# Kernel tuning notes

Measured on AMD Instinct MI355X. Metric: run time of the kernel, lower is better.

Reference implementation:

```python
import jax, jax.numpy as jnp
import numpy as np

DIM = 1024
HEADS = 16
HEAD_DIM = DIM // HEADS
HIDDEN = 4096
EPS = 1e-5


def _layer_norm(x, w, b):
    mu = jnp.mean(x, axis=-1, keepdims=True)
    var = jnp.var(x, axis=-1, keepdims=True)
    return (x - mu) * jax.lax.rsqrt(var + EPS) * w + b


def setup_inputs() -> dict:
    key = jax.random.key(0)
    ks = jax.random.split(key, 16)
    s = lambda fan_in: 1.0 / np.sqrt(fan_in)
    return {
        "x": jax.random.normal(ks[0], (8, 1024, DIM), dtype=jnp.float32),
        "ln1_w": jnp.ones((DIM,), jnp.float32),
        "ln1_b": jnp.zeros((DIM,), jnp.float32),
        "qkv_w": jax.random.uniform(ks[1], (3 * DIM, DIM), jnp.float32, -s(DIM), s(DIM)),
        "qkv_b": jax.random.uniform(ks[2], (3 * DIM,), jnp.float32, -s(DIM), s(DIM)),
        "out_w": jax.random.uniform(ks[3], (DIM, DIM), jnp.float32, -s(DIM), s(DIM)),
        "out_b": jax.random.uniform(ks[4], (DIM,), jnp.float32, -s(DIM), s(DIM)),
        "ln2_w": jnp.ones((DIM,), jnp.float32),
        "ln2_b": jnp.zeros((DIM,), jnp.float32),
        "fc1_w": jax.random.uniform(ks[5], (HIDDEN, DIM), jnp.float32, -s(DIM), s(DIM)),
        "fc1_b": jax.random.uniform(ks[6], (HIDDEN,), jnp.float32, -s(DIM), s(DIM)),
        "fc2_w": jax.random.uniform(ks[7], (DIM, HIDDEN), jnp.float32, -s(HIDDEN), s(HIDDEN)),
        "fc2_b": jax.random.uniform(ks[8], (DIM,), jnp.float32, -s(HIDDEN), s(HIDDEN)),
    }


def reference(x, ln1_w, ln1_b, qkv_w, qkv_b, out_w, out_b,
              ln2_w, ln2_b, fc1_w, fc1_b, fc2_w, fc2_b):
    B, S, D = x.shape
    # --- attention sub-block (pre-LN) ---
    h = _layer_norm(x, ln1_w, ln1_b)
    qkv = h @ qkv_w.T + qkv_b                              # [B,S,3D]
    qkv = qkv.reshape(B, S, 3, HEADS, HEAD_DIM)
    q, k, v = qkv[:, :, 0], qkv[:, :, 1], qkv[:, :, 2]     # [B,S,H,hd]
    scores = jnp.einsum('bqhd,bkhd->bhqk', q, k) / np.sqrt(HEAD_DIM)
    attn = jax.nn.softmax(scores, axis=-1)
    o = jnp.einsum('bhqk,bkhd->bqhd', attn, v).reshape(B, S, D)
    x = x + (o @ out_w.T + out_b)
    # --- MLP sub-block (pre-LN) ---
    h = _layer_norm(x, ln2_w, ln2_b)
    h = jax.nn.gelu(h @ fc1_w.T + fc1_b, approximate=False)
    x = x + (h @ fc2_w.T + fc2_b)
    return x
```

## Files before the change

kernel.cpp:

```cpp
#include <hip/hip_runtime.h>
#include <hip/hip_bf16.h>

typedef unsigned short u16;
typedef __bf16 bf16x8 __attribute__((ext_vector_type(8)));
typedef float f32x4 __attribute__((ext_vector_type(4)));
typedef u16 u16x8 __attribute__((ext_vector_type(8)));
typedef unsigned u32x2 __attribute__((ext_vector_type(2)));

#define LOG2E 1.4426950408889634f
#define QSCALE 0.18033688011112042f

template <int V> struct ic { static constexpr int v = V; };

__device__ __forceinline__ float fast_exp2(float x) {
#if __has_builtin(__builtin_amdgcn_exp2f)
  return __builtin_amdgcn_exp2f(x);
#else
  return exp2f(x);
#endif
}

__device__ __forceinline__ u16 f2bf(float f) {
  union { float f; unsigned u; } c; c.f = f;
  unsigned r = c.u + 0x7fffu + ((c.u >> 16) & 1u);
  return (u16)(r >> 16);
}

__device__ __forceinline__ unsigned pk_bf16(float a, float b) {
#if __has_builtin(__builtin_amdgcn_cvt_pk_bf16_f32)
  typedef __bf16 bf16x2_t __attribute__((ext_vector_type(2)));
  union { bf16x2_t v; unsigned u; } c;
  c.v = __builtin_amdgcn_cvt_pk_bf16_f32(a, b);
  return c.u;
#else
  return (unsigned)f2bf(a) | ((unsigned)f2bf(b) << 16);
#endif
}

__device__ __forceinline__ unsigned pk_bf16_fast(float a, float b) {
#if __has_builtin(__builtin_amdgcn_cvt_pk_bf16_f32)
  return pk_bf16(a, b);
#else
  union { float f; unsigned u; } ca, cb;
  ca.f = a; cb.f = b;
  return __builtin_amdgcn_perm(cb.u, ca.u, 0x07060302u);
#endif
}

__device__ __forceinline__ float gelu_f(float v) {
  float z = 0.7978845608f * v + 0.0356774081f * (v * v * v);
  float e = fast_exp2(z * 2.885390082f);
  float t = 1.0f - 2.0f * __builtin_amdgcn_rcpf(e + 1.0f);
  return 0.5f * v * (1.0f + t);
}

__device__ __forceinline__ void async16(const void* g, void* l) {
  __builtin_amdgcn_global_load_lds(
      (const __attribute__((address_space(1))) void*)g,
      (__attribute__((address_space(3))) void*)l, 16, 0, 0);
}

#define CFENCE asm volatile("" ::: "memory")
#define VMCNT(N) do { asm volatile("s_waitcnt vmcnt(" #N ")" ::: "memory"); \
                      __builtin_amdgcn_sched_barrier(0); } while (0)

__global__ __launch_bounds__(256) void cvt4_kernel(
    const float* __restrict__ s0, const float* __restrict__ s1,
    const float* __restrict__ s2, const float* __restrict__ s3,
    u16* __restrict__ d0, u16* __restrict__ d1,
    u16* __restrict__ d2, u16* __restrict__ d3) {
  int i = blockIdx.x * 256 + threadIdx.x;
  const float* s; u16* d; int off;
  if (i < 786432)       { s = s0; d = d0; off = i; }
  else if (i < 1048576) { s = s1; d = d1; off = i - 786432; }
  else if (i < 2097152) { s = s2; d = d2; off = i - 1048576; }
  else                  { s = s3; d = d3; off = i - 2097152; }
  float4 v = ((const float4*)s)[off];
  ushort4 o;
  o.x = f2bf(v.x); o.y = f2bf(v.y); o.z = f2bf(v.z); o.w = f2bf(v.w);
  ((ushort4*)d)[off] = o;
}

__global__ __launch_bounds__(256) void ln_kernel(const float* __restrict__ x,
                                                 const float* __restrict__ w,
                                                 const float* __restrict__ b,
                                                 u16* __restrict__ out) {
  int row = blockIdx.x;
  int tid = threadIdx.x;
  int lane = tid & 63, wave = tid >> 6;
  float4 v = ((const float4*)(x + (size_t)row * 1024))[tid];
  float s = v.x + v.y + v.z + v.w;
  float s2 = v.x*v.x + v.y*v.y + v.z*v.z + v.w*v.w;
  #pragma unroll
  for (int off = 1; off < 64; off <<= 1) {
    s += __shfl_xor(s, off, 64);
    s2 += __shfl_xor(s2, off, 64);
  }
  __shared__ float red[8];
  if (lane == 0) { red[wave] = s; red[4 + wave] = s2; }
  __syncthreads();
  float st = red[0] + red[1] + red[2] + red[3];
  float s2t = red[4] + red[5] + red[6] + red[7];
  float mu = st * (1.0f / 1024.0f);
  float var = s2t * (1.0f / 1024.0f) - mu * mu;
  float rs = rsqrtf(var + 1e-5f);
  float4 wv = ((const float4*)w)[tid];
  float4 bv = ((const float4*)b)[tid];
  ushort4 o;
  o.x = f2bf((v.x - mu) * rs * wv.x + bv.x);
  o.y = f2bf((v.y - mu) * rs * wv.y + bv.y);
  o.z = f2bf((v.z - mu) * rs * wv.z + bv.z);
  o.w = f2bf((v.w - mu) * rs * wv.w + bv.w);
  ((ushort4*)(out + (size_t)row * 1024))[tid] = o;
}

template <int EPI, int BM, int BN, int NBLOG2>
__global__ __launch_bounds__(512, 2) void gemm8(const u16* __restrict__ A,
                                                const u16* __restrict__ B,
                                                const float* __restrict__ bias,
                                                void* __restrict__ Cout,
                                                const float* __restrict__ resid,
                                                int M, int N, int K) {
  (void)M;
  constexpr int FMH = BM / 64;
  constexpr int FNH = BN / 128;
  constexpr int LA = BM / 128;
  constexpr int LB = BN / 128;
  constexpr int STEADY = LA + LB;
  __shared__ u16 As[2][BM * 64];
  __shared__ u16 Bs[2][BN * 64];
  const int tid = threadIdx.x;
  const int lane = tid & 63, wave = tid >> 6;
  const int wr = wave & 1, wc = wave >> 1;
  const int l15 = lane & 15, l4 = lane >> 4;
  const int nt = K >> 6;

  int m0, n0;
  if constexpr (NBLOG2 < 0) {
    m0 = blockIdx.y * BM; n0 = blockIdx.x * BN;
  } else {
    const int id = blockIdx.x;
    const int xcd = id & 7, slot = id >> 3;
    m0 = ((slot >> NBLOG2) * 8 + xcd) * BM;
    n0 = (slot & ((1 << NBLOG2) - 1)) * BN;
  }

  const int srow = lane >> 3;
  const int sg = (lane & 7) ^ srow;
  const u16* Ab = A + (size_t)(m0 + srow) * K + sg * 8;
  const u16* Bb = B + (size_t)(n0 + srow) * K + sg * 8;

  auto stageA = [&](int tile, int half, int wb) {
    if (tile >= nt) return;
    #pragma unroll
    for (int t = 0; t < LA; t++) {
      const int r0 = half * (BM / 2) + wave * (BM / 16) + t * 8;
      async16(Ab + (size_t)r0 * K + tile * 64, &As[wb][r0 * 64]);
    }
  };
  auto stageB = [&](int tile, int half, int wb) {
    if (tile >= nt) return;
    #pragma unroll
    for (int t = 0; t < LB; t++) {
      const int r0 = half * (BN / 2) + wave * (BN / 16) + t * 8;
      async16(Bb + (size_t)r0 * K + tile * 64, &Bs[wb][r0 * 64]);
    }
  };

  f32x4 acc[2][FMH][2][FNH];
  #pragma unroll
  for (int a = 0; a < 2; a++)
    #pragma unroll
    for (int f = 0; f < FMH; f++)
      #pragma unroll
      for (int c = 0; c < 2; c++)
        #pragma unroll
        for (int g = 0; g < FNH; g++) {
          f32x4 z = {0.f, 0.f, 0.f, 0.f};
          acc[a][f][c][g] = z;
        }

  auto phase = [&](auto qa_, auto qb_, int rb, auto stage) {
    constexpr int qa = decltype(qa_)::v;
    constexpr int qb = decltype(qb_)::v;
    bf16x8 af[FMH][2], bfr[FNH][2];
    #pragma unroll
    for (int f = 0; f < FMH; f++)
      #pragma unroll
      for (int ks = 0; ks < 2; ks++) {
        const int row = qa * (BM / 2) + wr * (BM / 4) + f * 16 + l15;
        const int sl = (ks * 4 + l4) ^ (l15 & 7);
        af[f][ks] = *(const bf16x8*)&As[rb][row * 64 + sl * 8];
      }
    #pragma unroll
    for (int f = 0; f < FNH; f++)
      #pragma unroll
      for (int ks = 0; ks < 2; ks++) {
        const int col = qb * (BN / 2) + wc * (BN / 8) + f * 16 + l15;
        const int sl = (ks * 4 + l4) ^ (l15 & 7);
        bfr[f][ks] = *(const bf16x8*)&Bs[rb][col * 64 + sl * 8];
      }
    stage();
    CFENCE;
    __builtin_amdgcn_s_barrier();
    asm volatile("s_waitcnt lgkmcnt(0)" ::: "memory");
    __builtin_amdgcn_sched_barrier(0);
    __builtin_amdgcn_s_setprio(1);
    #pragma unroll
    for (int f = 0; f < FMH; f++)
      #pragma unroll
      for (int g = 0; g < FNH; g++)
        #pragma unroll
        for (int ks = 0; ks < 2; ks++)
          acc[qa][f][qb][g] = __builtin_amdgcn_mfma_f32_16x16x32_bf16(
              af[f][ks], bfr[g][ks], acc[qa][f][qb][g], 0, 0, 0);
    __builtin_amdgcn_s_setprio(0);
    __builtin_amdgcn_sched_barrier(0);
  };

  auto endphase = [&](int mode) {
    if (mode == 1) {
      if constexpr (STEADY == 4) VMCNT(4); else VMCNT(3);
    } else if (mode == 2) {
      VMCNT(0);
    }
    CFENCE;
    __builtin_amdgcn_s_barrier();
  };

  stageA(0, 0, 0); stageB(0, 0, 0); stageA(0, 1, 0); stageB(0, 1, 0);
  stageA(1, 0, 1); stageB(1, 0, 1);
  if constexpr (STEADY == 4) VMCNT(4); else VMCNT(3);
  CFENCE;
  __builtin_amdgcn_s_barrier();

  const int niter = nt >> 1;
  for (int it = 0; it < niter; ++it) {
    const int T = 2 * it;
    const int f4 = (T + 2 < nt) ? 1 : 2;
    const int f8 = (T + 3 < nt) ? 1 : 2;
    phase(ic<0>{}, ic<0>{}, 0, [&]{ stageA(T + 1, 1, 1); }); endphase(0);
    phase(ic<0>{}, ic<1>{}, 0, [&]{ stageB(T + 1, 1, 1); }); endphase(0);
    phase(ic<1>{}, ic<0>{}, 0, [&]{ stageA(T + 2, 0, 0); }); endphase(0);
    phase(ic<1>{}, ic<1>{}, 0, [&]{ stageB(T + 2, 0, 0); }); endphase(f4);
    phase(ic<0>{}, ic<0>{}, 1, [&]{ stageA(T + 2, 1, 0); }); endphase(0);
    phase(ic<0>{}, ic<1>{}, 1, [&]{ stageB(T + 2, 1, 0); }); endphase(0);
    phase(ic<1>{}, ic<0>{}, 1, [&]{ stageA(T + 3, 0, 1); }); endphase(0);
    phase(ic<1>{}, ic<1>{}, 1, [&]{ stageB(T + 3, 0, 1); }); endphase(f8);
  }

  float bv[2][FNH];
  #pragma unroll
  for (int qb = 0; qb < 2; qb++)
    #pragma unroll
    for (int fn = 0; fn < FNH; fn++)
      bv[qb][fn] = bias[n0 + qb * (BN / 2) + wc * (BN / 8) + fn * 16 + l15];

  #pragma unroll
  for (int qa = 0; qa < 2; qa++)
    #pragma unroll
    for (int fm = 0; fm < FMH; fm++) {
      const size_t row0 =
          (size_t)(m0 + qa * (BM / 2) + wr * (BM / 4) + fm * 16 + l4 * 4);
      #pragma unroll
      for (int r = 0; r < 4; r += 2)
        #pragma unroll
        for (int qb = 0; qb < 2; qb++)
          #pragma unroll
          for (int fn = 0; fn < FNH; fn++) {
            const int col = n0 + qb * (BN / 2) + wc * (BN / 8) + fn * 16 + l15;
            float v0 = acc[qa][fm][qb][fn][r] + bv[qb][fn];
            float v1 = acc[qa][fm][qb][fn][r + 1] + bv[qb][fn];
            if (EPI == 1) { v0 = gelu_f(v0); v1 = gelu_f(v1); }
            if (EPI == 3) {
              float sc = (col < 1024) ? QSCALE : 1.0f;
              v0 *= sc; v1 *= sc;
            }
            const size_t off0 = (row0 + r) * (size_t)N + col;
            const size_t off1 = (row0 + r + 1) * (size_t)N + col;
            if (EPI == 2) {
              ((float*)Cout)[off0] = v0 + resid[off0];
              ((float*)Cout)[off1] = v1 + resid[off1];
            } else {
              unsigned pk = pk_bf16(v0, v1);
              ((u16*)Cout)[off0] = (u16)pk;
              ((u16*)Cout)[off1] = (u16)(pk >> 16);
            }
          }
    }
}

__global__ __launch_bounds__(256) void vtrans_kernel(const u16* __restrict__ qkv,
                                                     u16* __restrict__ vtg) {
  const int sc = blockIdx.x, h = blockIdx.y, b = blockIdx.z;
  const int tid = threadIdx.x;
  __shared__ u16 t[64][72];
  const u16* vp = qkv + ((size_t)b * 1024) * 3072 + h * 64 + 2048;
  #pragma unroll
  for (int it = 0; it < 2; it++) {
    int idx = it * 256 + tid;
    int row = idx >> 3, g = idx & 7;
    *(u16x8*)&t[row][g * 8] =
        *(const u16x8*)(vp + (size_t)(sc * 64 + row) * 3072 + g * 8);
  }
  __syncthreads();
  u16* dst = vtg + ((size_t)(b * 16 + h) * 64) * 1024;
  #pragma unroll
  for (int it = 0; it < 2; it++) {
    int idx = it * 256 + tid;
    int d = idx >> 3, g = idx & 7;
    u16x8 o;
    #pragma unroll
    for (int j = 0; j < 8; j++) o[j] = t[g * 8 + j][d];
    *(u16x8*)(dst + (size_t)d * 1024 + sc * 64 + g * 8) = o;
  }
}

__global__ __launch_bounds__(256) void attn_kernel(const u16* __restrict__ qkv,
                                                   const u16* __restrict__ vtg,
                                                   u16* __restrict__ obuf) {
  const int S = 1024, QKV = 3072;
  const int id = blockIdx.x;
  const int qt = id >> 7, hb = id & 127;
  const int h = hb & 15, b = hb >> 4;
  const int tid = threadIdx.x, lane = tid & 63, wave = tid >> 6;
  const int l15 = lane & 15, l4 = lane >> 4;
  const size_t tok0 = (size_t)b * S;
  const u16* qp = qkv + tok0 * QKV + h * 64;
  const u16* kp = qp + 1024;
  const u16* vtp = vtg + (size_t)(b * 16 + h) * 64 * 1024;
  const int q0 = qt * 128;

  __shared__ u16 Ks[128 * 64];
  __shared__ u16 Vt[64 * 128];
  __shared__ u16 Ps[4][16 * 136];

  const u16* qrow = qp + (size_t)(q0 + wave * 16 + l15) * QKV;
  bf16x8 qf[2][2];
  #pragma unroll
  for (int qs = 0; qs < 2; qs++)
    #pragma unroll
    for (int kb = 0; kb < 2; kb++)
      qf[qs][kb] = *(const bf16x8*)(qrow + (size_t)qs * 64 * QKV + kb * 32 + l4 * 8);

  bf16x8 ones;
  #pragma unroll
  for (int j = 0; j < 8; j++) ones[j] = (__bf16)1.0f;

  const int krow = lane >> 3;
  const int klg = (lane & 7) ^ (lane >> 3);
  const int vrow_i = lane >> 4;
  const int vpg = lane & 15;

  f32x4 oacc[2][4], lacc[2];
  #pragma unroll
  for (int qs = 0; qs < 2; qs++) {
    #pragma unroll
    for (int ct = 0; ct < 4; ct++) {
      f32x4 z = {0.f, 0.f, 0.f, 0.f};
      oacc[qs][ct] = z;
    }
    f32x4 z = {0.f, 0.f, 0.f, 0.f};
    lacc[qs] = z;
  }

  for (int j0 = 0; j0 < S; j0 += 128) {
    __syncthreads();
    #pragma unroll
    for (int t = 0; t < 4; t++) {
      int e = wave * 4 + t;
      async16(kp + (size_t)(j0 + e * 8 + krow) * QKV + klg * 8, Ks + e * 512);
    }
    #pragma unroll
    for (int t = 0; t < 4; t++) {
      int e = wave * 4 + t;
      int row = e * 4 + vrow_i;
      int lg = vpg ^ (row & 15);
      async16(vtp + (size_t)row * 1024 + j0 + lg * 8, Vt + e * 512);
    }
    __syncthreads();

    #pragma unroll
    for (int qs = 0; qs < 2; qs++) {
      f32x4 s[8];
      #pragma unroll
      for (int tg = 0; tg < 8; tg++) {
        f32x4 z = {0.f, 0.f, 0.f, 0.f};
        s[tg] = z;
        #pragma unroll
        for (int kb = 0; kb < 2; kb++) {
          int pg = (kb * 4 + l4) ^ (l15 & 7);
          bf16x8 kf = *(const bf16x8*)&Ks[(tg * 16 + l15) * 64 + pg * 8];
          s[tg] = __builtin_amdgcn_mfma_f32_16x16x32_bf16(kf, qf[qs][kb], s[tg], 0, 0, 0);
        }
      }

      #pragma unroll
      for (int tg = 0; tg < 8; tg++)
        #pragma unroll
        for (int r = 0; r < 4; r++)
          s[tg][r] = fast_exp2(s[tg][r]);

      #pragma unroll
      for (int tg = 0; tg < 8; tg++) {
        u32x2 pr;
        pr[0] = pk_bf16_fast(s[tg][0], s[tg][1]);
        pr[1] = pk_bf16_fast(s[tg][2], s[tg][3]);
        *(u32x2*)&Ps[wave][l15 * 136 + tg * 16 + l4 * 4] = pr;
      }
      bf16x8 pf[4];
      #pragma unroll
      for (int kb = 0; kb < 4; kb++)
        pf[kb] = *(const bf16x8*)&Ps[wave][l15 * 136 + kb * 32 + l4 * 8];

      #pragma unroll
      for (int kb = 0; kb < 4; kb++) {
        #pragma unroll
        for (int ct = 0; ct < 4; ct++) {
          int pg = (kb * 4 + l4) ^ l15;
          bf16x8 vf = *(const bf16x8*)&Vt[(ct * 16 + l15) * 128 + pg * 8];
          oacc[qs][ct] = __builtin_amdgcn_mfma_f32_16x16x32_bf16(
              pf[kb], vf, oacc[qs][ct], 0, 0, 0);
        }
        lacc[qs] = __builtin_amdgcn_mfma_f32_16x16x32_bf16(
            pf[kb], ones, lacc[qs], 0, 0, 0);
      }
    }
  }

  #pragma unroll
  for (int qs = 0; qs < 2; qs++) {
    float inv[4];
    #pragma unroll
    for (int r = 0; r < 4; r++) inv[r] = 1.0f / lacc[qs][r];
    #pragma unroll
    for (int ct = 0; ct < 4; ct++)
      #pragma unroll
      for (int r = 0; r < 4; r++) {
        float v = oacc[qs][ct][r] * inv[r];
        size_t row = tok0 + q0 + qs * 64 + wave * 16 + l4 * 4 + r;
        obuf[row * 1024 + h * 64 + ct * 16 + l15] = f2bf(v);
      }
  }
}

extern "C" void kernel_launch(void* const* d_in, const int* in_sizes, int n_in,
                              void* d_out, int out_size, void* d_ws, size_t ws_size,
                              hipStream_t stream) {
  (void)in_sizes; (void)n_in; (void)out_size; (void)ws_size;
  const float* x     = (const float*)d_in[0];
  const float* ln1_w = (const float*)d_in[1];
  const float* ln1_b = (const float*)d_in[2];
  const float* qkv_w = (const float*)d_in[3];
  const float* qkv_b = (const float*)d_in[4];
  const float* out_w = (const float*)d_in[5];
  const float* out_b = (const float*)d_in[6];
  const float* ln2_w = (const float*)d_in[7];
  const float* ln2_b = (const float*)d_in[8];
  const float* fc1_w = (const float*)d_in[9];
  const float* fc1_b = (const float*)d_in[10];
  const float* fc2_w = (const float*)d_in[11];
  const float* fc2_b = (const float*)d_in[12];
  float* out = (float*)d_out;

  char* ws = (char*)d_ws;
  u16* wqkv = (u16*)(ws);
  u16* wout = (u16*)(ws + 6291456);
  u16* wfc1 = (u16*)(ws + 8388608);
  u16* wfc2 = (u16*)(ws + 16777216);
  u16* hbuf = (u16*)(ws + 25165824);
  u16* qbuf = (u16*)(ws + 41943040);
  u16* vtg  = (u16*)(ws + 92274688);

  const int M = 8192;

  cvt4_kernel<<<dim3(12288), 256, 0, stream>>>(qkv_w, out_w, fc1_w, fc2_w,
                                               wqkv, wout, wfc1, wfc2);

  ln_kernel<<<dim3(M), 256, 0, stream>>>(x, ln1_w, ln1_b, hbuf);
  gemm8<3, 128, 256, -1><<<dim3(3072 / 256, M / 128), 512, 0, stream>>>(
      hbuf, wqkv, qkv_b, qbuf, nullptr, M, 3072, 1024);
  vtrans_kernel<<<dim3(16, 16, 8), 256, 0, stream>>>(qbuf, vtg);
  attn_kernel<<<dim3(1024), 256, 0, stream>>>(qbuf, vtg, hbuf);
  gemm8<2, 128, 256, -1><<<dim3(1024 / 256, M / 128), 512, 0, stream>>>(
      hbuf, wout, out_b, out, x, M, 1024, 1024);
  ln_kernel<<<dim3(M), 256, 0, stream>>>(out, ln2_w, ln2_b, hbuf);
  gemm8<1, 256, 256, -1><<<dim3(4096 / 256, M / 256), 512, 0, stream>>>(
      hbuf, wfc1, fc1_b, qbuf, nullptr, M, 4096, 1024);
  gemm8<2, 128, 256, 2><<<dim3((M / 128) * (1024 / 256)), 512, 0, stream>>>(
      qbuf, wfc2, fc2_b, out, out, M, 1024, 4096);
}
```

Measured before the change: 527.6 us.

## Prefetch LDS fragments into registers one phase ahead in GEMM main loop

Restructures the 8-phase GEMM loop so A and B register fragments are read from LDS one phase ahead into double-buffered register arrays. Each phase then waits only on the older LDS reads (partial lgkmcnt) before issuing MFMAs, letting LDS reads overlap with matrix math. The vmcnt waits are moved to the phase before each buffer switch. This raises register pressure and makes the wait-count bookkeeping fragile.

```diff
diff --git a/kernel.cpp b/kernel.cpp
--- a/kernel.cpp
+++ b/kernel.cpp
@@ -63,6 +63,15 @@
 #define CFENCE asm volatile("" ::: "memory")
 #define VMCNT(N) do { asm volatile("s_waitcnt vmcnt(" #N ")" ::: "memory"); \
                       __builtin_amdgcn_sched_barrier(0); } while (0)
+
+template <int N> __device__ __forceinline__ void lgkm() {
+  if constexpr (N == 0)       asm volatile("s_waitcnt lgkmcnt(0)" ::: "memory");
+  else if constexpr (N == 4)  asm volatile("s_waitcnt lgkmcnt(4)" ::: "memory");
+  else if constexpr (N == 8)  asm volatile("s_waitcnt lgkmcnt(8)" ::: "memory");
+  else if constexpr (N == 12) asm volatile("s_waitcnt lgkmcnt(12)" ::: "memory");
+  else                        asm volatile("s_waitcnt lgkmcnt(0)" ::: "memory");
+  __builtin_amdgcn_sched_barrier(0);
+}
 
 __global__ __launch_bounds__(256) void cvt4_kernel(
     const float* __restrict__ s0, const float* __restrict__ s1,
@@ -126,7 +135,6 @@
   constexpr int FNH = BN / 128;
   constexpr int LA = BM / 128;
   constexpr int LB = BN / 128;
-  constexpr int STEADY = LA + LB;
   __shared__ u16 As[2][BM * 64];
   __shared__ u16 Bs[2][BN * 64];
   const int tid = threadIdx.x;
@@ -167,6 +175,30 @@
     }
   };
 
+  bf16x8 aA[FMH][2], aB[FMH][2];
+  bf16x8 b0r[FNH][2], b1r[FNH][2];
+
+  auto loadAto = [&](bf16x8 (&dst)[FMH][2], const u16* buf, int half) {
+    #pragma unroll
+    for (int f = 0; f < FMH; f++)
+      #pragma unroll
+      for (int ks = 0; ks < 2; ks++) {
+        const int row = half * (BM / 2) + wr * (BM / 4) + f * 16 + l15;
+        const int sl = (ks * 4 + l4) ^ (l15 & 7);
+        dst[f][ks] = *(const bf16x8*)&buf[row * 64 + sl * 8];
+      }
+  };
+  auto loadBto = [&](bf16x8 (&dst)[FNH][2], const u16* buf, int half) {
+    #pragma unroll
+    for (int f = 0; f < FNH; f++)
+      #pragma unroll
+      for (int ks = 0; ks < 2; ks++) {
+        const int col = half * (BN / 2) + wc * (BN / 8) + f * 16 + l15;
+        const int sl = (ks * 4 + l4) ^ (l15 & 7);
+        dst[f][ks] = *(const bf16x8*)&buf[col * 64 + sl * 8];
+      }
+  };
+
   f32x4 acc[2][FMH][2][FNH];
   #pragma unroll
   for (int a = 0; a < 2; a++)
@@ -180,31 +212,15 @@
           acc[a][f][c][g] = z;
         }
 
-  auto phase = [&](auto qa_, auto qb_, int rb, auto stage) {
+  auto phase = [&](auto qa_, auto qb_, auto& Aarr, auto& Barr, auto lg_,
+                   auto pf, auto stg, auto endv_) {
     constexpr int qa = decltype(qa_)::v;
     constexpr int qb = decltype(qb_)::v;
-    bf16x8 af[FMH][2], bfr[FNH][2];
-    #pragma unroll
-    for (int f = 0; f < FMH; f++)
-      #pragma unroll
-      for (int ks = 0; ks < 2; ks++) {
-        const int row = qa * (BM / 2) + wr * (BM / 4) + f * 16 + l15;
-        const int sl = (ks * 4 + l4) ^ (l15 & 7);
-        af[f][ks] = *(const bf16x8*)&As[rb][row * 64 + sl * 8];
-      }
-    #pragma unroll
-    for (int f = 0; f < FNH; f++)
-      #pragma unroll
-      for (int ks = 0; ks < 2; ks++) {
-        const int col = qb * (BN / 2) + wc * (BN / 8) + f * 16 + l15;
-        const int sl = (ks * 4 + l4) ^ (l15 & 7);
-        bfr[f][ks] = *(const bf16x8*)&Bs[rb][col * 64 + sl * 8];
-      }
-    stage();
+    pf();
+    stg();
     CFENCE;
     __builtin_amdgcn_s_barrier();
-    asm volatile("s_waitcnt lgkmcnt(0)" ::: "memory");
-    __builtin_amdgcn_sched_barrier(0);
+    lgkm<decltype(lg_)::v>();
     __builtin_amdgcn_s_setprio(1);
     #pragma unroll
     for (int f = 0; f < FMH; f++)
@@ -213,16 +229,11 @@
         #pragma unroll
         for (int ks = 0; ks < 2; ks++)
           acc[qa][f][qb][g] = __builtin_amdgcn_mfma_f32_16x16x32_bf16(
-              af[f][ks], bfr[g][ks], acc[qa][f][qb][g], 0, 0, 0);
+              Aarr[f][ks], Barr[g][ks], acc[qa][f][qb][g], 0, 0, 0);
     __builtin_amdgcn_s_setprio(0);
     __builtin_amdgcn_sched_barrier(0);
-  };
-
-  auto endphase = [&](int mode) {
-    if (mode == 1) {
-      if constexpr (STEADY == 4) VMCNT(4); else VMCNT(3);
-    } else if (mode == 2) {
-      VMCNT(0);
+    if constexpr (decltype(endv_)::v == 1) {
+      if constexpr (LA == 1) VMCNT(1); else VMCNT(2);
     }
     CFENCE;
     __builtin_amdgcn_s_barrier();
@@ -230,24 +241,45 @@
 
   stageA(0, 0, 0); stageB(0, 0, 0); stageA(0, 1, 0); stageB(0, 1, 0);
   stageA(1, 0, 1); stageB(1, 0, 1);
-  if constexpr (STEADY == 4) VMCNT(4); else VMCNT(3);
+  if constexpr (LA + LB == 4) VMCNT(4); else VMCNT(3);
   CFENCE;
   __builtin_amdgcn_s_barrier();
+  loadAto(aA, &As[0][0], 0);
+  loadBto(b0r, &Bs[0][0], 0);
+
+  constexpr int C_B = 2 * FNH;
+  constexpr int C_A = 2 * FMH;
+  constexpr int C_AB = C_A + C_B;
 
   const int niter = nt >> 1;
   for (int it = 0; it < niter; ++it) {
     const int T = 2 * it;
-    const int f4 = (T + 2 < nt) ? 1 : 2;
-    const int f8 = (T + 3 < nt) ? 1 : 2;
-    phase(ic<0>{}, ic<0>{}, 0, [&]{ stageA(T + 1, 1, 1); }); endphase(0);
-    phase(ic<0>{}, ic<1>{}, 0, [&]{ stageB(T + 1, 1, 1); }); endphase(0);
-    phase(ic<1>{}, ic<0>{}, 0, [&]{ stageA(T + 2, 0, 0); }); endphase(0);
-    phase(ic<1>{}, ic<1>{}, 0, [&]{ stageB(T + 2, 0, 0); }); endphase(f4);
-    phase(ic<0>{}, ic<0>{}, 1, [&]{ stageA(T + 2, 1, 0); }); endphase(0);
-    phase(ic<0>{}, ic<1>{}, 1, [&]{ stageB(T + 2, 1, 0); }); endphase(0);
-    phase(ic<1>{}, ic<0>{}, 1, [&]{ stageA(T + 3, 0, 1); }); endphase(0);
-    phase(ic<1>{}, ic<1>{}, 1, [&]{ stageB(T + 3, 0, 1); }); endphase(f8);
-  }
+    phase(ic<0>{}, ic<0>{}, aA, b0r, ic<C_B>{},
+          [&]{ loadBto(b1r, &Bs[0][0], 1); },
+          [&]{ stageA(T + 1, 1, 1); }, ic<0>{});
+    phase(ic<0>{}, ic<1>{}, aA, b1r, ic<C_A>{},
+          [&]{ loadAto(aB, &As[0][0], 1); },
+          [&]{ stageB(T + 1, 1, 1); }, ic<0>{});
+    phase(ic<1>{}, ic<0>{}, aB, b0r, ic<0>{},
+          [&]{},
+          [&]{ stageA(T + 2, 0, 0); }, ic<1>{});
+    phase(ic<1>{}, ic<1>{}, aB, b1r, ic<C_AB>{},
+          [&]{ loadAto(aA, &As[1][0], 0); loadBto(b0r, &Bs[1][0], 0); },
+          [&]{ stageB(T + 2, 0, 0); }, ic<0>{});
+    phase(ic<0>{}, ic<0>{}, aA, b0r, ic<C_B>{},
+          [&]{ loadBto(b1r, &Bs[1][0], 1); },
+          [&]{ stageA(T + 2, 1, 0); }, ic<0>{});
+    phase(ic<0>{}, ic<1>{}, aA, b1r, ic<C_A>{},
+          [&]{ loadAto(aB, &As[1][0], 1); },
+          [&]{ stageB(T + 2, 1, 0); }, ic<0>{});
+    phase(ic<1>{}, ic<0>{}, aB, b0r, ic<0>{},
+          [&]{},
+          [&]{ stageA(T + 3, 0, 1); }, ic<1>{});
+    phase(ic<1>{}, ic<1>{}, aB, b1r, ic<C_AB>{},
+          [&]{ loadAto(aA, &As[0][0], 0); loadBto(b0r, &Bs[0][0], 0); },
+          [&]{ stageB(T + 3, 0, 1); }, ic<0>{});
+  }
+  VMCNT(0);
 
   float bv[2][FNH];
   #pragma unroll
```

Result: slower. 557.5 us (+5.7%).
